# Kernel tuning notes

Measured on AMD Instinct MI355X. Metric: run time of the kernel, lower is better.

Reference implementation:

```python
import jax, jax.numpy as jnp
import numpy as np

B, S, D, H = 2048, 200, 128, 4
H1, H2 = 64, 32
F = 4 * D
TIME_DECAY = 0.1


def setup_inputs() -> dict:
    key = jax.random.key(0)
    ks = jax.random.split(key, 10)
    query = jax.random.normal(ks[0], (B, D), dtype=jnp.float32)
    keys = jax.random.normal(ks[1], (B, S, D), dtype=jnp.float32)
    keys_mask = jax.random.randint(ks[2], (B, S), 0, 2).astype(bool)
    keys_mask = keys_mask.at[:, 0].set(True)  # avoid fully-masked rows
    sc = 0.02
    # per-head MLP params, stacked over heads
    W1 = sc * jax.random.normal(ks[3], (H, H1, F), dtype=jnp.float32)
    b1 = jnp.zeros((H, H1), dtype=jnp.float32)
    a1 = 0.25 * jnp.ones((H,), dtype=jnp.float32)  # PReLU (default single param)
    W2 = sc * jax.random.normal(ks[4], (H, H2, H1), dtype=jnp.float32)
    b2 = jnp.zeros((H, H2), dtype=jnp.float32)
    a2 = 0.25 * jnp.ones((H,), dtype=jnp.float32)
    W3 = sc * jax.random.normal(ks[5], (H, H2), dtype=jnp.float32)
    b3 = jnp.zeros((H,), dtype=jnp.float32)
    Wo = sc * jax.random.normal(ks[6], (D, D), dtype=jnp.float32)
    bo = jnp.zeros((D,), dtype=jnp.float32)
    return {"query": query, "keys": keys, "keys_mask": keys_mask,
            "W1": W1, "b1": b1, "a1": a1, "W2": W2, "b2": b2, "a2": a2,
            "W3": W3, "b3": b3, "Wo": Wo, "bo": bo}


def reference(query, keys, keys_mask, W1, b1, a1, W2, b2, a2, W3, b3, Wo, bo):
    b, s, d = keys.shape
    q = query[:, None, :]                                    # [B,1,D]
    x = jnp.concatenate(
        [keys, jnp.broadcast_to(q, (b, s, d)), keys * q, keys - q], axis=-1)  # [B,S,4D]
    pos = jnp.arange(s, dtype=keys.dtype)
    tw = jnp.exp(TIME_DECAY * (pos - s + 1))                 # [S]
    # all heads batched: [B,H,S,H1]
    h = jnp.einsum('bsf,hdf->bhsd', x, W1) + b1[None, :, None, :]
    h = jnp.where(h >= 0, h, a1[None, :, None, None] * h)    # PReLU
    h = jnp.einsum('bhsd,hed->bhse', h, W2) + b2[None, :, None, :]
    h = jnp.where(h >= 0, h, a2[None, :, None, None] * h)
    scores = jnp.einsum('bhse,he->bhs', h, W3) + b3[None, :, None]
    scores = scores * tw[None, None, :]
    scores = jnp.where(keys_mask[:, None, :], scores, -1e9)
    w = jax.nn.softmax(scores, axis=-1)                      # [B,H,S]
    out_h = jnp.einsum('bhs,bsd->bhd', w, keys)              # [B,H,D]
    combined = out_h.mean(axis=1)                            # [B,D]
    output = combined @ Wo.T + bo                            # [B,D]
    avg_weights = w.mean(axis=1)                             # [B,S]
    return output, avg_weights
```

## Files before the change

kernel.cpp:

```cpp
#include <hip/hip_runtime.h>
#include <hip/hip_bf16.h>
#include <stdint.h>

#define Bsz 2048
#define Ssz 200
#define Dsz 128
#define Hsz 4
#define SP  224
#define SPB 232

typedef __attribute__((ext_vector_type(8))) short short8;
typedef __attribute__((ext_vector_type(4))) float f32x4;
typedef unsigned short ushort_t;
typedef unsigned int uint_t;

#define KEYS_OFF   0
#define W1H_OFF    57344
#define W2S_OFF    122880
#define SCW_OFF    139264
#define SCWB_OFF   142848
#define C1S_OFF    150272
#define QS_OFF     151296
#define B2S_OFF    151808
#define W3S_OFF    152320
#define MASK_OFF   152832
#define COMB_OFF   153728
#define PO_OFF     154240
#define A1S_OFF    156288
#define A2S_OFF    156304
#define B3S_OFF    156320
#define SMEM_BYTES 156336

__device__ __forceinline__ ushort_t f2bf(float x) {
    union { float f; uint_t u; } v; v.f = x;
    uint_t u = v.u;
    u += 0x7FFFu + ((u >> 16) & 1u);
    return (ushort_t)(u >> 16);
}

__global__ void prep_kernel(const float* __restrict__ W1, const float* __restrict__ W2,
                            const float* __restrict__ Wo,
                            float* __restrict__ W1sum, float* __restrict__ W1c,
                            float* __restrict__ W1diffT, float* __restrict__ WoT,
                            ushort_t* __restrict__ W2bf) {
    int i = blockIdx.x * blockDim.x + threadIdx.x;
    if (i < 32768) {
        int n = i >> 7, j = i & 127;
        float a  = W1[n * 512 + j];
        float dd = W1[n * 512 + 384 + j];
        W1sum[i] = a + dd;
        W1c[i]   = W1[n * 512 + 256 + j];
        W1diffT[j * 256 + n] = W1[n * 512 + 128 + j] - dd;
    }
    if (i < 16384) {
        int j = i >> 7, d = i & 127;
        WoT[i] = Wo[d * 128 + j];
    }
    if (i < 8192) W2bf[i] = f2bf(W2[i]);
}

__global__ void c1_kernel(const float* __restrict__ query, const float* __restrict__ W1diffT,
                          const float* __restrict__ b1, float* __restrict__ c1out) {
    __shared__ float qs[128];
    int b = blockIdx.x, t = threadIdx.x;
    if (t < 128) qs[t] = query[b * 128 + t];
    __syncthreads();
    float acc = b1[t];
    #pragma unroll 8
    for (int j = 0; j < 128; ++j) acc += W1diffT[j * 256 + t] * qs[j];
    c1out[b * 256 + t] = acc;
}

__launch_bounds__(512, 1)
__global__ void attn_kernel(const float* __restrict__ query, const float* __restrict__ keys,
                            const int* __restrict__ kmask,
                            const float* __restrict__ a1, const float* __restrict__ b2,
                            const float* __restrict__ a2, const float* __restrict__ W3,
                            const float* __restrict__ b3, const float* __restrict__ bo,
                            const float* __restrict__ W1sum, const float* __restrict__ W1c,
                            const float* __restrict__ WoT, const ushort_t* __restrict__ W2bf,
                            const float* __restrict__ c1ws, float* __restrict__ out) {
    extern __shared__ char smem[];
    const int tid = threadIdx.x;
    const int bb  = blockIdx.x;
    const int w   = tid >> 6;
    const int l   = tid & 63;
    const int l15 = l & 15;
    const int lk  = l >> 4;

    float* qs   = (float*)(smem + QS_OFF);
    float* b2s  = (float*)(smem + B2S_OFF);
    float* w3s  = (float*)(smem + W3S_OFF);
    float* c1s  = (float*)(smem + C1S_OFF);
    float* scw  = (float*)(smem + SCW_OFF);
    int*   mks  = (int*)(smem + MASK_OFF);
    float* comb = (float*)(smem + COMB_OFF);
    float* po   = (float*)(smem + PO_OFF);
    float* a1s  = (float*)(smem + A1S_OFF);
    float* a2s  = (float*)(smem + A2S_OFF);
    float* b3s  = (float*)(smem + B3S_OFF);

    if (tid < 128) qs[tid] = query[bb * 128 + tid];
    else if (tid < 256) b2s[tid - 128] = b2[tid - 128];
    else if (tid < 384) w3s[tid - 256] = W3[tid - 256];
    else if (tid < 396) {
        int i = tid - 384;
        if (i < 4) a1s[i] = a1[i];
        else if (i < 8) a2s[i - 4] = a2[i - 4];
        else b3s[i - 8] = b3[i - 8];
    }
    if (tid < SP)  mks[tid] = (tid < Ssz) ? kmask[bb * Ssz + tid] : 0;
    if (tid < 256) c1s[tid] = c1ws[bb * 256 + tid];
    {
        uint_t* zb = (uint_t*)(smem + SCWB_OFF);
        for (int i = tid; i < 1856; i += 512) zb[i] = 0;
    }
    __syncthreads();

    #pragma unroll
    for (int it = 0; it < 14; ++it) {
        int id = tid + 512 * it;
        int row = id >> 5, c4 = id & 31;
        float4 kv = {0.f, 0.f, 0.f, 0.f};
        if (row < Ssz) kv = *(const float4*)(keys + (size_t)(bb * Ssz + row) * Dsz + c4 * 4);
        uint_t p0 = (uint_t)f2bf(kv.x) | ((uint_t)f2bf(kv.y) << 16);
        uint_t p1 = (uint_t)f2bf(kv.z) | ((uint_t)f2bf(kv.w) << 16);
        int off = KEYS_OFF + (((row << 8) + (c4 << 3)) ^ ((row & 7) << 4));
        *(uint_t*)(smem + off)     = p0;
        *(uint_t*)(smem + off + 4) = p1;
    }
    const uint_t* W2u = (const uint_t*)W2bf;
    #pragma unroll
    for (int it = 0; it < 8; ++it) {
        int p = tid + 512 * it;
        int flat = p * 2;
        int h = flat >> 11, rem = flat & 2047;
        int e = rem >> 6, k = rem & 63;
        int off = W2S_OFF + ((((h << 12) + (e << 7) + (k << 1))) ^ ((e & 7) << 4));
        *(uint_t*)(smem + off) = W2u[p];
    }
    const float2* Ws2 = (const float2*)W1sum;
    const float2* Wc2 = (const float2*)W1c;
    #pragma unroll
    for (int it = 0; it < 32; ++it) {
        int p = tid + 512 * it;
        int n = p >> 6, jp = p & 63;
        float2 sv = Ws2[p];
        float2 cv = Wc2[p];
        float q0 = qs[jp * 2], q1 = qs[jp * 2 + 1];
        uint_t pk = (uint_t)f2bf(sv.x + cv.x * q0) | ((uint_t)f2bf(sv.y + cv.y * q1) << 16);
        int off = W1H_OFF + ((((n << 8) + (jp << 2))) ^ ((n & 7) << 4));
        *(uint_t*)(smem + off) = pk;
    }
    __syncthreads();

    const int wr = w >> 2;
    const int wc = w & 3;
    const f32x4 fz = {0.f, 0.f, 0.f, 0.f};
    f32x4 acc[7][4];
    #pragma unroll
    for (int m = 0; m < 7; ++m)
        #pragma unroll
        for (int n = 0; n < 4; ++n) acc[m][n] = fz;

    #pragma unroll
    for (int t = 0; t < 4; ++t) {
        short8 bfr[4];
        #pragma unroll
        for (int nt = 0; nt < 4; ++nt) {
            int n = wc * 64 + nt * 16 + l15;
            int off = W1H_OFF + ((((n << 8) + (t * 64 + lk * 16))) ^ ((n & 7) << 4));
            bfr[nt] = *(const short8*)(smem + off);
        }
        #pragma unroll
        for (int mt = 0; mt < 7; ++mt) {
            int gmt = wr * 7 + mt;
            if (gmt < 13) {
                int row = gmt * 16 + l15;
                int off = KEYS_OFF + ((((row << 8) + (t * 64 + lk * 16))) ^ ((row & 7) << 4));
                short8 afr = *(const short8*)(smem + off);
                #pragma unroll
                for (int nt = 0; nt < 4; ++nt)
                    acc[mt][nt] = __builtin_amdgcn_mfma_f32_16x16x32_bf16(afr, bfr[nt], acc[mt][nt], 0, 0, 0);
            }
        }
    }
    __syncthreads();

    float c1v[4];
    #pragma unroll
    for (int nt = 0; nt < 4; ++nt) c1v[nt] = c1s[wc * 64 + nt * 16 + l15];
    const float a1v = a1s[wc];
    const int h2 = w >> 1;
    float b2v[2], w3v[2];
    #pragma unroll
    for (int nt = 0; nt < 2; ++nt) {
        b2v[nt] = b2s[h2 * 32 + nt * 16 + l15];
        w3v[nt] = w3s[h2 * 32 + nt * 16 + l15];
    }
    const float a2v = a2s[h2];
    const float b3v = b3s[h2];

    #pragma unroll
    for (int c = 0; c < 2; ++c) {
        const int TT = (c == 0) ? 7 : 6;
        if (wr == c) {
            #pragma unroll
            for (int mt = 0; mt < 7; ++mt) {
                if (mt < TT) {
                    int rbase = mt * 16 + lk * 4;
                    #pragma unroll
                    for (int nt = 0; nt < 4; ++nt) {
                        int n = wc * 64 + nt * 16 + l15;
                        #pragma unroll
                        for (int r = 0; r < 4; ++r) {
                            float v = acc[mt][nt][r] + c1v[nt];
                            v = (v >= 0.f) ? v : a1v * v;
                            int lrow = rbase + r;
                            int off = W1H_OFF + ((((lrow << 9) + (n << 1))) ^ ((lrow & 7) << 4));
                            *(ushort_t*)(smem + off) = f2bf(v);
                        }
                    }
                }
            }
        }
        __syncthreads();
        for (int t2 = (w & 1); t2 < TT; t2 += 2) {
            f32x4 acc2[2];
            acc2[0] = fz; acc2[1] = fz;
            #pragma unroll
            for (int kt = 0; kt < 2; ++kt) {
                int lrow = t2 * 16 + l15;
                int k = kt * 32 + lk * 8;
                int aoff = W1H_OFF + ((((lrow << 9) + ((h2 * 64 + k) << 1))) ^ ((lrow & 7) << 4));
                short8 afr = *(const short8*)(smem + aoff);
                #pragma unroll
                for (int nt = 0; nt < 2; ++nt) {
                    int e = nt * 16 + l15;
                    int boff = W2S_OFF + ((((h2 << 12) + (e << 7) + (k << 1))) ^ ((e & 7) << 4));
                    short8 bfr2 = *(const short8*)(smem + boff);
                    acc2[nt] = __builtin_amdgcn_mfma_f32_16x16x32_bf16(afr, bfr2, acc2[nt], 0, 0, 0);
                }
            }
            #pragma unroll
            for (int r = 0; r < 4; ++r) {
                float sum = 0.f;
                #pragma unroll
                for (int nt = 0; nt < 2; ++nt) {
                    float v = acc2[nt][r] + b2v[nt];
                    v = (v >= 0.f) ? v : a2v * v;
                    sum += v * w3v[nt];
                }
                sum += __shfl_xor(sum, 1);
                sum += __shfl_xor(sum, 2);
                sum += __shfl_xor(sum, 4);
                sum += __shfl_xor(sum, 8);
                if (l15 == 0) {
                    int sg = c * 112 + t2 * 16 + lk * 4 + r;
                    float tw = __expf(0.1f * (float)(sg - (Ssz - 1)));
                    float sc = (sum + b3v) * tw;
                    scw[h2 * SP + sg] = mks[sg] ? sc : -1.0e9f;
                }
            }
        }
        __syncthreads();
    }

    if (w < 4) {
        float xv[4], ex[4];
        float mx = -3.0e38f;
        #pragma unroll
        for (int i = 0; i < 4; ++i) {
            int s = l + 64 * i;
            xv[i] = (s < Ssz) ? scw[w * SP + s] : -1.0e30f;
            mx = fmaxf(mx, xv[i]);
        }
        #pragma unroll
        for (int m = 1; m < 64; m <<= 1) mx = fmaxf(mx, __shfl_xor(mx, m));
        float sm = 0.f;
        #pragma unroll
        for (int i = 0; i < 4; ++i) {
            int s = l + 64 * i;
            ex[i] = (s < Ssz) ? __expf(xv[i] - mx) : 0.f;
            sm += ex[i];
        }
        #pragma unroll
        for (int m = 1; m < 64; m <<= 1) sm += __shfl_xor(sm, m);
        float inv = 1.0f / sm;
        #pragma unroll
        for (int i = 0; i < 4; ++i) {
            int s = l + 64 * i;
            float wv = ex[i] * inv;
            if (s < SP) scw[w * SP + s] = wv;
            if (s < SPB) *(ushort_t*)(smem + SCWB_OFF + w * (SPB * 2) + s * 2) = f2bf(wv);
        }
    }
    __syncthreads();

    if (tid < Ssz) {
        float aw = 0.25f * (scw[tid] + scw[SP + tid] + scw[2 * SP + tid] + scw[3 * SP + tid]);
        out[Bsz * Dsz + bb * Ssz + tid] = aw;
    }

    f32x4 acc4 = fz;
    #pragma unroll
    for (int t = 0; t < 7; ++t) {
        int k0 = t * 32 + lk * 8;
        short8 afr = *(const short8*)(smem + SCWB_OFF + l15 * (SPB * 2) + k0 * 2);
        short8 bfr;
        #pragma unroll
        for (int j = 0; j < 8; ++j) {
            int srow = k0 + j;
            int off = KEYS_OFF + ((((srow << 8) + ((16 * w + l15) << 1))) ^ ((srow & 7) << 4));
            bfr[j] = *(const short*)(smem + off);
        }
        acc4 = __builtin_amdgcn_mfma_f32_16x16x32_bf16(afr, bfr, acc4, 0, 0, 0);
    }
    if (lk == 0) comb[16 * w + l15] = 0.25f * (acc4[0] + acc4[1] + acc4[2] + acc4[3]);
    __syncthreads();

    {
        int d = tid & 127, part = tid >> 7;
        float o = 0.f;
        const float* wp = WoT + (size_t)part * 32 * 128 + d;
        #pragma unroll 8
        for (int j = 0; j < 32; ++j) o += comb[part * 32 + j] * wp[j * 128];
        po[part * 128 + d] = o;
    }
    __syncthreads();
    if (tid < Dsz) {
        out[bb * Dsz + tid] = bo[tid] + po[tid] + po[128 + tid] + po[256 + tid] + po[384 + tid];
    }
}

extern "C" void kernel_launch(void* const* d_in, const int* in_sizes, int n_in,
                              void* d_out, int out_size, void* d_ws, size_t ws_size,
                              hipStream_t stream) {
    const float* query = (const float*)d_in[0];
    const float* keys  = (const float*)d_in[1];
    const int*   kmask = (const int*)d_in[2];
    const float* W1    = (const float*)d_in[3];
    const float* b1    = (const float*)d_in[4];
    const float* a1    = (const float*)d_in[5];
    const float* W2    = (const float*)d_in[6];
    const float* b2    = (const float*)d_in[7];
    const float* a2    = (const float*)d_in[8];
    const float* W3    = (const float*)d_in[9];
    const float* b3    = (const float*)d_in[10];
    const float* Wo    = (const float*)d_in[11];
    const float* bo    = (const float*)d_in[12];
    float* out = (float*)d_out;

    char* ws = (char*)d_ws;
    float*    W1sum   = (float*)(ws);
    float*    W1c     = (float*)(ws + 131072);
    float*    W1diffT = (float*)(ws + 262144);
    float*    WoT     = (float*)(ws + 393216);
    ushort_t* W2bf    = (ushort_t*)(ws + 458752);
    float*    c1ws    = (float*)(ws + 475136);

    hipFuncSetAttribute(reinterpret_cast<const void*>(attn_kernel),
                        hipFuncAttributeMaxDynamicSharedMemorySize, SMEM_BYTES);

    prep_kernel<<<128, 256, 0, stream>>>(W1, W2, Wo, W1sum, W1c, W1diffT, WoT, W2bf);
    c1_kernel<<<Bsz, 256, 0, stream>>>(query, W1diffT, b1, c1ws);
    attn_kernel<<<Bsz, 512, SMEM_BYTES, stream>>>(query, keys, kmask, a1, b2, a2, W3, b3, bo,
                                                  W1sum, W1c, WoT, W2bf, c1ws, out);
}
```

Before: 225.4 us.

## Cut LDS footprint by streaming keys and W1 from global, fuse c1 into attention

Keys and the query-folded W1 are no longer staged in shared memory as bf16. Each wave now loads them from global memory per K-step, converts to bf16 in registers and feeds MFMA, processing the sequence in two row halves with smaller accumulators. This shrinks LDS from about 156KB to about 67KB and raises launch bounds so several blocks can share a CU. The separate c1 kernel is folded into the attention kernel, and the weighted key sum becomes a plain fp32 loop over global keys. The trade is redundant global/L2 traffic and repeated conversion of keys and W1 across waves in exchange for occupancy and one fewer launch.

```diff
diff --git a/kernel.cpp b/kernel.cpp
--- a/kernel.cpp
+++ b/kernel.cpp
@@ -7,29 +7,25 @@
 #define Dsz 128
 #define Hsz 4
 #define SP  224
-#define SPB 232
 
 typedef __attribute__((ext_vector_type(8))) short short8;
 typedef __attribute__((ext_vector_type(4))) float f32x4;
 typedef unsigned short ushort_t;
 typedef unsigned int uint_t;
 
-#define KEYS_OFF   0
-#define W1H_OFF    57344
-#define W2S_OFF    122880
-#define SCW_OFF    139264
-#define SCWB_OFF   142848
-#define C1S_OFF    150272
-#define QS_OFF     151296
-#define B2S_OFF    151808
-#define W3S_OFF    152320
-#define MASK_OFF   152832
-#define COMB_OFF   153728
-#define PO_OFF     154240
-#define A1S_OFF    156288
-#define A2S_OFF    156304
-#define B3S_OFF    156320
-#define SMEM_BYTES 156336
+#define H1C_OFF    0
+#define SCW_OFF    57344
+#define C1S_OFF    60928
+#define QS_OFF     61952
+#define B2S_OFF    62464
+#define W3S_OFF    62976
+#define MASK_OFF   63488
+#define COMB_OFF   64384
+#define PO_OFF     64896
+#define A1S_OFF    66944
+#define A2S_OFF    66960
+#define B3S_OFF    66976
+#define SMEM_BYTES 66992
 
 __device__ __forceinline__ ushort_t f2bf(float x) {
     union { float f; uint_t u; } v; v.f = x;
@@ -59,27 +55,17 @@
     if (i < 8192) W2bf[i] = f2bf(W2[i]);
 }
 
-__global__ void c1_kernel(const float* __restrict__ query, const float* __restrict__ W1diffT,
-                          const float* __restrict__ b1, float* __restrict__ c1out) {
-    __shared__ float qs[128];
-    int b = blockIdx.x, t = threadIdx.x;
-    if (t < 128) qs[t] = query[b * 128 + t];
-    __syncthreads();
-    float acc = b1[t];
-    #pragma unroll 8
-    for (int j = 0; j < 128; ++j) acc += W1diffT[j * 256 + t] * qs[j];
-    c1out[b * 256 + t] = acc;
-}
-
-__launch_bounds__(512, 1)
+__launch_bounds__(512, 4)
 __global__ void attn_kernel(const float* __restrict__ query, const float* __restrict__ keys,
                             const int* __restrict__ kmask,
                             const float* __restrict__ a1, const float* __restrict__ b2,
                             const float* __restrict__ a2, const float* __restrict__ W3,
-                            const float* __restrict__ b3, const float* __restrict__ bo,
+                            const float* __restrict__ b3, const float* __restrict__ b1,
+                            const float* __restrict__ bo,
                             const float* __restrict__ W1sum, const float* __restrict__ W1c,
+                            const float* __restrict__ W1diffT,
                             const float* __restrict__ WoT, const ushort_t* __restrict__ W2bf,
-                            const float* __restrict__ c1ws, float* __restrict__ out) {
+                            float* __restrict__ out) {
     extern __shared__ char smem[];
     const int tid = threadIdx.x;
     const int bb  = blockIdx.x;
@@ -101,97 +87,40 @@
     float* b3s  = (float*)(smem + B3S_OFF);
 
     if (tid < 128) qs[tid] = query[bb * 128 + tid];
-    else if (tid < 256) b2s[tid - 128] = b2[tid - 128];
-    else if (tid < 384) w3s[tid - 256] = W3[tid - 256];
-    else if (tid < 396) {
-        int i = tid - 384;
+    else if (tid < 256) {
+        int i = tid - 128;
+        if (i < Hsz * 32) b2s[i] = b2[i];
+    }
+    if (tid >= 480 && tid < 492) {
+        int i = tid - 480;
         if (i < 4) a1s[i] = a1[i];
         else if (i < 8) a2s[i - 4] = a2[i - 4];
         else b3s[i - 8] = b3[i - 8];
     }
     if (tid < SP)  mks[tid] = (tid < Ssz) ? kmask[bb * Ssz + tid] : 0;
-    if (tid < 256) c1s[tid] = c1ws[bb * 256 + tid];
-    {
-        uint_t* zb = (uint_t*)(smem + SCWB_OFF);
-        for (int i = tid; i < 1856; i += 512) zb[i] = 0;
-    }
-    __syncthreads();
-
-    #pragma unroll
-    for (int it = 0; it < 14; ++it) {
-        int id = tid + 512 * it;
-        int row = id >> 5, c4 = id & 31;
-        float4 kv = {0.f, 0.f, 0.f, 0.f};
-        if (row < Ssz) kv = *(const float4*)(keys + (size_t)(bb * Ssz + row) * Dsz + c4 * 4);
-        uint_t p0 = (uint_t)f2bf(kv.x) | ((uint_t)f2bf(kv.y) << 16);
-        uint_t p1 = (uint_t)f2bf(kv.z) | ((uint_t)f2bf(kv.w) << 16);
-        int off = KEYS_OFF + (((row << 8) + (c4 << 3)) ^ ((row & 7) << 4));
-        *(uint_t*)(smem + off)     = p0;
-        *(uint_t*)(smem + off + 4) = p1;
-    }
-    const uint_t* W2u = (const uint_t*)W2bf;
-    #pragma unroll
-    for (int it = 0; it < 8; ++it) {
-        int p = tid + 512 * it;
-        int flat = p * 2;
-        int h = flat >> 11, rem = flat & 2047;
-        int e = rem >> 6, k = rem & 63;
-        int off = W2S_OFF + ((((h << 12) + (e << 7) + (k << 1))) ^ ((e & 7) << 4));
-        *(uint_t*)(smem + off) = W2u[p];
-    }
-    const float2* Ws2 = (const float2*)W1sum;
-    const float2* Wc2 = (const float2*)W1c;
-    #pragma unroll
-    for (int it = 0; it < 32; ++it) {
-        int p = tid + 512 * it;
-        int n = p >> 6, jp = p & 63;
-        float2 sv = Ws2[p];
-        float2 cv = Wc2[p];
-        float q0 = qs[jp * 2], q1 = qs[jp * 2 + 1];
-        uint_t pk = (uint_t)f2bf(sv.x + cv.x * q0) | ((uint_t)f2bf(sv.y + cv.y * q1) << 16);
-        int off = W1H_OFF + ((((n << 8) + (jp << 2))) ^ ((n & 7) << 4));
-        *(uint_t*)(smem + off) = pk;
-    }
-    __syncthreads();
-
-    const int wr = w >> 2;
-    const int wc = w & 3;
+    if (tid >= 256 && tid < 384) w3s[tid - 256] = W3[tid - 256];
+    if (tid >= 256) {
+        int n = tid - 256;
+        float acc0 = b1[n], acc1 = 0.f;
+        #pragma unroll 4
+        for (int j = 0; j < 128; j += 2) {
+            acc0 += W1diffT[j * 256 + n] * query[bb * 128 + j];
+            acc1 += W1diffT[(j + 1) * 256 + n] * query[bb * 128 + j + 1];
+        }
+        c1s[n] = acc0 + acc1;
+    }
+    __syncthreads();
+
+    const int wr = w & 1;
+    const int wc = w >> 1;
+    const int h2 = w >> 1;
+    const int mtl = w & 1;
     const f32x4 fz = {0.f, 0.f, 0.f, 0.f};
-    f32x4 acc[7][4];
-    #pragma unroll
-    for (int m = 0; m < 7; ++m)
-        #pragma unroll
-        for (int n = 0; n < 4; ++n) acc[m][n] = fz;
-
-    #pragma unroll
-    for (int t = 0; t < 4; ++t) {
-        short8 bfr[4];
-        #pragma unroll
-        for (int nt = 0; nt < 4; ++nt) {
-            int n = wc * 64 + nt * 16 + l15;
-            int off = W1H_OFF + ((((n << 8) + (t * 64 + lk * 16))) ^ ((n & 7) << 4));
-            bfr[nt] = *(const short8*)(smem + off);
-        }
-        #pragma unroll
-        for (int mt = 0; mt < 7; ++mt) {
-            int gmt = wr * 7 + mt;
-            if (gmt < 13) {
-                int row = gmt * 16 + l15;
-                int off = KEYS_OFF + ((((row << 8) + (t * 64 + lk * 16))) ^ ((row & 7) << 4));
-                short8 afr = *(const short8*)(smem + off);
-                #pragma unroll
-                for (int nt = 0; nt < 4; ++nt)
-                    acc[mt][nt] = __builtin_amdgcn_mfma_f32_16x16x32_bf16(afr, bfr[nt], acc[mt][nt], 0, 0, 0);
-            }
-        }
-    }
-    __syncthreads();
 
     float c1v[4];
     #pragma unroll
     for (int nt = 0; nt < 4; ++nt) c1v[nt] = c1s[wc * 64 + nt * 16 + l15];
     const float a1v = a1s[wc];
-    const int h2 = w >> 1;
     float b2v[2], w3v[2];
     #pragma unroll
     for (int nt = 0; nt < 2; ++nt) {
@@ -201,46 +130,99 @@
     const float a2v = a2s[h2];
     const float b3v = b3s[h2];
 
-    #pragma unroll
-    for (int c = 0; c < 2; ++c) {
-        const int TT = (c == 0) ? 7 : 6;
-        if (wr == c) {
-            #pragma unroll
-            for (int mt = 0; mt < 7; ++mt) {
-                if (mt < TT) {
-                    int rbase = mt * 16 + lk * 4;
+    #pragma unroll 1
+    for (int p = 0; p < 2; ++p) {
+        const int TT = (p == 0) ? 7 : 6;
+        f32x4 acc[4][4];
+        #pragma unroll
+        for (int i = 0; i < 4; ++i)
+            #pragma unroll
+            for (int n = 0; n < 4; ++n) acc[i][n] = fz;
+
+        #pragma unroll 1
+        for (int t = 0; t < 4; ++t) {
+            const int k0 = 32 * t + 8 * lk;
+            float qv[8];
+            #pragma unroll
+            for (int j = 0; j < 8; ++j) qv[j] = qs[k0 + j];
+            short8 bfr[4];
+            #pragma unroll
+            for (int nt = 0; nt < 4; ++nt) {
+                int n = wc * 64 + nt * 16 + l15;
+                const float4* ps = (const float4*)(W1sum + n * 128 + k0);
+                const float4* pc = (const float4*)(W1c + n * 128 + k0);
+                float4 s0 = ps[0], s1 = ps[1];
+                float4 c0 = pc[0], c1f = pc[1];
+                bfr[nt][0] = (short)f2bf(s0.x + c0.x * qv[0]);
+                bfr[nt][1] = (short)f2bf(s0.y + c0.y * qv[1]);
+                bfr[nt][2] = (short)f2bf(s0.z + c0.z * qv[2]);
+                bfr[nt][3] = (short)f2bf(s0.w + c0.w * qv[3]);
+                bfr[nt][4] = (short)f2bf(s1.x + c1f.x * qv[4]);
+                bfr[nt][5] = (short)f2bf(s1.y + c1f.y * qv[5]);
+                bfr[nt][6] = (short)f2bf(s1.z + c1f.z * qv[6]);
+                bfr[nt][7] = (short)f2bf(s1.w + c1f.w * qv[7]);
+            }
+            #pragma unroll
+            for (int i = 0; i < 4; ++i) {
+                int lt = 2 * i + wr;
+                if (lt < TT) {
+                    int grow = p * 112 + lt * 16 + l15;
+                    int rowc = (grow < Ssz) ? grow : (Ssz - 1);
+                    const float4* pk = (const float4*)(keys + (size_t)(bb * Ssz + rowc) * Dsz + k0);
+                    float4 k0v = pk[0], k1v = pk[1];
+                    short8 afr;
+                    afr[0] = (short)f2bf(k0v.x); afr[1] = (short)f2bf(k0v.y);
+                    afr[2] = (short)f2bf(k0v.z); afr[3] = (short)f2bf(k0v.w);
+                    afr[4] = (short)f2bf(k1v.x); afr[5] = (short)f2bf(k1v.y);
+                    afr[6] = (short)f2bf(k1v.z); afr[7] = (short)f2bf(k1v.w);
                     #pragma unroll
-                    for (int nt = 0; nt < 4; ++nt) {
-                        int n = wc * 64 + nt * 16 + l15;
-                        #pragma unroll
-                        for (int r = 0; r < 4; ++r) {
-                            float v = acc[mt][nt][r] + c1v[nt];
-                            v = (v >= 0.f) ? v : a1v * v;
-                            int lrow = rbase + r;
-                            int off = W1H_OFF + ((((lrow << 9) + (n << 1))) ^ ((lrow & 7) << 4));
-                            *(ushort_t*)(smem + off) = f2bf(v);
-                        }
+                    for (int nt = 0; nt < 4; ++nt)
+                        acc[i][nt] = __builtin_amdgcn_mfma_f32_16x16x32_bf16(afr, bfr[nt], acc[i][nt], 0, 0, 0);
+                }
+            }
+        }
+
+        #pragma unroll
+        for (int i = 0; i < 4; ++i) {
+            int lt = 2 * i + wr;
+            if (lt < TT) {
+                #pragma unroll
+                for (int nt = 0; nt < 4; ++nt) {
+                    int n = wc * 64 + nt * 16 + l15;
+                    #pragma unroll
+                    for (int r = 0; r < 4; ++r) {
+                        float v = acc[i][nt][r] + c1v[nt];
+                        v = (v >= 0.f) ? v : a1v * v;
+                        int lrow = lt * 16 + lk * 4 + r;
+                        int off = H1C_OFF + ((((lrow << 9) + (n << 1))) ^ ((lrow & 7) << 4));
+                        *(ushort_t*)(smem + off) = f2bf(v);
                     }
                 }
             }
         }
         __syncthreads();
-        for (int t2 = (w & 1); t2 < TT; t2 += 2) {
+
+        short8 w2f[2][2];
+        #pragma unroll
+        for (int kt = 0; kt < 2; ++kt)
+            #pragma unroll
+            for (int nt = 0; nt < 2; ++nt) {
+                int e = nt * 16 + l15;
+                int kk = kt * 32 + lk * 8;
+                w2f[kt][nt] = *(const short8*)(W2bf + h2 * 2048 + e * 64 + kk);
+            }
+        for (int t2 = mtl; t2 < TT; t2 += 2) {
             f32x4 acc2[2];
             acc2[0] = fz; acc2[1] = fz;
             #pragma unroll
             for (int kt = 0; kt < 2; ++kt) {
                 int lrow = t2 * 16 + l15;
-                int k = kt * 32 + lk * 8;
-                int aoff = W1H_OFF + ((((lrow << 9) + ((h2 * 64 + k) << 1))) ^ ((lrow & 7) << 4));
+                int kk = kt * 32 + lk * 8;
+                int aoff = H1C_OFF + ((((lrow << 9) + ((h2 * 64 + kk) << 1))) ^ ((lrow & 7) << 4));
                 short8 afr = *(const short8*)(smem + aoff);
                 #pragma unroll
-                for (int nt = 0; nt < 2; ++nt) {
-                    int e = nt * 16 + l15;
-                    int boff = W2S_OFF + ((((h2 << 12) + (e << 7) + (k << 1))) ^ ((e & 7) << 4));
-                    short8 bfr2 = *(const short8*)(smem + boff);
-                    acc2[nt] = __builtin_amdgcn_mfma_f32_16x16x32_bf16(afr, bfr2, acc2[nt], 0, 0, 0);
-                }
+                for (int nt = 0; nt < 2; ++nt)
+                    acc2[nt] = __builtin_amdgcn_mfma_f32_16x16x32_bf16(afr, w2f[kt][nt], acc2[nt], 0, 0, 0);
             }
             #pragma unroll
             for (int r = 0; r < 4; ++r) {
@@ -256,7 +238,7 @@
                 sum += __shfl_xor(sum, 4);
                 sum += __shfl_xor(sum, 8);
                 if (l15 == 0) {
-                    int sg = c * 112 + t2 * 16 + lk * 4 + r;
+                    int sg = p * 112 + t2 * 16 + lk * 4 + r;
                     float tw = __expf(0.1f * (float)(sg - (Ssz - 1)));
                     float sc = (sum + b3v) * tw;
                     scw[h2 * SP + sg] = mks[sg] ? sc : -1.0e9f;
@@ -290,9 +272,7 @@
         #pragma unroll
         for (int i = 0; i < 4; ++i) {
             int s = l + 64 * i;
-            float wv = ex[i] * inv;
-            if (s < SP) scw[w * SP + s] = wv;
-            if (s < SPB) *(ushort_t*)(smem + SCWB_OFF + w * (SPB * 2) + s * 2) = f2bf(wv);
+            if (s < SP) scw[w * SP + s] = ex[i] * inv;
         }
     }
     __syncthreads();
@@ -302,21 +282,23 @@
         out[Bsz * Dsz + bb * Ssz + tid] = aw;
     }
 
-    f32x4 acc4 = fz;
-    #pragma unroll
-    for (int t = 0; t < 7; ++t) {
-        int k0 = t * 32 + lk * 8;
-        short8 afr = *(const short8*)(smem + SCWB_OFF + l15 * (SPB * 2) + k0 * 2);
-        short8 bfr;
-        #pragma unroll
-        for (int j = 0; j < 8; ++j) {
-            int srow = k0 + j;
-            int off = KEYS_OFF + ((((srow << 8) + ((16 * w + l15) << 1))) ^ ((srow & 7) << 4));
-            bfr[j] = *(const short*)(smem + off);
-        }
-        acc4 = __builtin_amdgcn_mfma_f32_16x16x32_bf16(afr, bfr, acc4, 0, 0, 0);
-    }
-    if (lk == 0) comb[16 * w + l15] = 0.25f * (acc4[0] + acc4[1] + acc4[2] + acc4[3]);
+    {
+        int h = tid >> 7, d = tid & 127;
+        const float* kb = keys + (size_t)bb * Ssz * Dsz + d;
+        const float* wrow = scw + h * SP;
+        float s0 = 0.f, s1 = 0.f, s2 = 0.f, s3 = 0.f;
+        #pragma unroll 2
+        for (int s = 0; s < Ssz; s += 4) {
+            s0 += wrow[s]     * kb[(size_t)s * Dsz];
+            s1 += wrow[s + 1] * kb[(size_t)(s + 1) * Dsz];
+            s2 += wrow[s + 2] * kb[(size_t)(s + 2) * Dsz];
+            s3 += wrow[s + 3] * kb[(size_t)(s + 3) * Dsz];
+        }
+        po[h * 128 + d] = 0.25f * ((s0 + s1) + (s2 + s3));
+    }
+    __syncthreads();
+
+    if (tid < Dsz) comb[tid] = po[tid] + po[128 + tid] + po[256 + tid] + po[384 + tid];
     __syncthreads();
 
     {
@@ -357,13 +339,11 @@
     float*    W1diffT = (float*)(ws + 262144);
     float*    WoT     = (float*)(ws + 393216);
     ushort_t* W2bf    = (ushort_t*)(ws + 458752);
-    float*    c1ws    = (float*)(ws + 475136);
 
     hipFuncSetAttribute(reinterpret_cast<const void*>(attn_kernel),
                         hipFuncAttributeMaxDynamicSharedMemorySize, SMEM_BYTES);
 
     prep_kernel<<<128, 256, 0, stream>>>(W1, W2, Wo, W1sum, W1c, W1diffT, WoT, W2bf);
-    c1_kernel<<<Bsz, 256, 0, stream>>>(query, W1diffT, b1, c1ws);
-    attn_kernel<<<Bsz, 512, SMEM_BYTES, stream>>>(query, keys, kmask, a1, b2, a2, W3, b3, bo,
-                                                  W1sum, W1c, WoT, W2bf, c1ws, out);
+    attn_kernel<<<Bsz, 512, SMEM_BYTES, stream>>>(query, keys, kmask, a1, b2, a2, W3, b3, b1, bo,
+                                                  W1sum, W1c, W1diffT, WoT, W2bf, out);
 }
```

Result: slower. 794.0 us (+252.2%).
